# Performance work log

Hardware: AMD Instinct MI355X
Metric: run time of the kernel (lower is better)

## Reference

```python
import jax, jax.numpy as jnp
import numpy as np

D, DC, DR, NH = 2048, 512, 64, 16
HD = D // NH
B, T = 2, 2048


def _rope_tables(sl, off, dr):
    inv = 1.0 / (10000.0 ** (jnp.arange(0, dr, 2, dtype=jnp.float32) / dr))
    t = jnp.arange(off, off + sl, dtype=jnp.float32)
    f = jnp.outer(t, inv)                      # [sl, dr/2]
    e = jnp.concatenate([f, f], -1)            # [sl, dr]
    return jnp.cos(e), jnp.sin(e)


def _rap(x, c, s):
    d = x.shape[-1]
    x1, x2 = x[..., : d // 2], x[..., d // 2:]
    ch, sh = c[..., : d // 2], s[..., : d // 2]
    return jnp.concatenate([x1 * ch - x2 * sh, x2 * ch + x1 * sh], -1)


def setup_inputs() -> dict:
    key = jax.random.key(0)
    ks = jax.random.split(key, 8)
    def w(k, i, o):
        return jax.random.normal(k, (i, o), jnp.float32) * (1.0 / np.sqrt(i))
    return {
        "x": jax.random.normal(ks[0], (B, T, D), jnp.float32),
        "Wkv": w(ks[1], D, DC),    # kv_down
        "Wkup": w(ks[2], DC, D),   # k_up
        "Wvup": w(ks[3], DC, D),   # v_up
        "Wq": w(ks[4], D, D),      # q_proj
        "Wqr": w(ks[5], D, DR),    # q_rope
        "Wkr": w(ks[6], DC, DR),   # k_rope
        "Wo": w(ks[7], D, D),      # o_proj
    }


def reference(x, Wkv, Wkup, Wvup, Wq, Wqr, Wkr, Wo):
    Bx, Tx, d = x.shape
    offset = 0
    ckv = x @ Wkv                                   # [B,T,dc]
    kr = ckv @ Wkr                                  # [B,T,dr]
    cos, sin = _rope_tables(Tx, offset, DR)         # [T,dr]
    kr = _rap(kr, cos[None], sin[None])
    entry = jnp.concatenate([ckv, kr], -1)          # [B,T,dc+dr] (kv cache entry)
    tl = entry.shape[1]

    k = (ckv @ Wkup).reshape(Bx, tl, NH, HD).transpose(0, 2, 1, 3)   # [B,H,tl,hd]
    v = (ckv @ Wvup).reshape(Bx, tl, NH, HD).transpose(0, 2, 1, 3)
    q = (x @ Wq).reshape(Bx, Tx, NH, HD).transpose(0, 2, 1, 3)        # [B,H,T,hd]

    qr = _rap(x @ Wqr, cos[None], sin[None])        # [B,T,dr]

    ac = jnp.einsum("bhtd,bhsd->bhts", q, k)        # content scores
    ar = jnp.einsum("btd,bsd->bts", qr, kr)         # shared RoPE scores (same per head)
    scale = np.sqrt(HD + DR).astype(np.float32)
    scores = (ac + ar[:, None]) / scale             # [B,H,T,tl]

    # causal mask: triu(-inf, diagonal=tl-T+1)
    i = jnp.arange(Tx)[:, None]
    j = jnp.arange(tl)[None, :]
    mask = j > i + (tl - Tx)
    scores = jnp.where(mask[None, None], -jnp.inf, scores)

    attn = jax.nn.softmax(scores, -1)
    out = jnp.einsum("bhts,bhsd->bhtd", attn, v).transpose(0, 2, 1, 3).reshape(Bx, Tx, -1)
    return out @ Wo, entry
```

## Files before the change

### kernel.cpp

```cpp
#include <hip/hip_runtime.h>
#include <math.h>
#include <type_traits>

#define D    2048
#define DC   512
#define DR   64
#define NH   16
#define HD   128
#define Bb   2
#define Tt   2048
#define ROWS (Bb*Tt)
#define LDX  2176

typedef __bf16 bf16x8 __attribute__((ext_vector_type(8)));
typedef __bf16 bf16x4 __attribute__((ext_vector_type(4)));
typedef float  f32x4  __attribute__((ext_vector_type(4)));
typedef float  f32x16 __attribute__((ext_vector_type(16)));
typedef unsigned int uint;

typedef const void __attribute__((address_space(1))) gvoid;
typedef void       __attribute__((address_space(3))) lvoid;

__device__ __forceinline__ void load_lds16(const void* g, void* l) {
    __builtin_amdgcn_global_load_lds((gvoid*)g, (lvoid*)l, 16, 0, 0);
}

template <bool WF32, bool WBF16>
__global__ __launch_bounds__(256)
void gemm_bt(const __bf16* __restrict__ A, const __bf16* __restrict__ BT,
             float* __restrict__ Cf, __bf16* __restrict__ Cb,
             int M, int K, int ldcf, int ldcb) {
    __shared__ __bf16 As[128 * 32];
    __shared__ __bf16 Bs[128 * 32];

    const int tid  = threadIdx.x;
    const int w    = tid >> 6;
    const int lane = tid & 63;
    const int quad = lane >> 4;
    const int lc   = lane & 15;
    const int bm   = blockIdx.y * 128;
    const int bn   = blockIdx.x * 128;
    const int wm   = (w & 1) * 64;
    const int wn   = (w >> 1) * 64;

    const int sr = w * 32 + (lane >> 2);
    const int sc = (lane & 3) * 8;

    f32x4 acc[4][4] = {};

    for (int k0 = 0; k0 < K; k0 += 32) {
        const __bf16* ga = A  + (size_t)(bm + sr) * K + k0 + sc;
        const __bf16* gb = BT + (size_t)(bn + sr) * K + k0 + sc;
        load_lds16(ga,                  &As[(w * 32) * 32]);
        load_lds16(ga + (size_t)16 * K, &As[(w * 32 + 16) * 32]);
        load_lds16(gb,                  &Bs[(w * 32) * 32]);
        load_lds16(gb + (size_t)16 * K, &Bs[(w * 32 + 16) * 32]);
        __syncthreads();

        bf16x8 af[4], bfr[4];
        #pragma unroll
        for (int mi = 0; mi < 4; ++mi)
            af[mi] = *(bf16x8*)&As[(wm + mi * 16 + lc) * 32 + quad * 8];
        #pragma unroll
        for (int ni = 0; ni < 4; ++ni)
            bfr[ni] = *(bf16x8*)&Bs[(wn + ni * 16 + lc) * 32 + quad * 8];
        #pragma unroll
        for (int mi = 0; mi < 4; ++mi)
            #pragma unroll
            for (int ni = 0; ni < 4; ++ni)
                acc[mi][ni] = __builtin_amdgcn_mfma_f32_16x16x32_bf16(
                    af[mi], bfr[ni], acc[mi][ni], 0, 0, 0);
        __syncthreads();
    }

    #pragma unroll
    for (int mi = 0; mi < 4; ++mi)
        #pragma unroll
        for (int r = 0; r < 4; ++r) {
            const int row = bm + wm + mi * 16 + quad * 4 + r;
            const int col = bn + wn + lc;
            #pragma unroll
            for (int ni = 0; ni < 4; ++ni) {
                float v = acc[mi][ni][r];
                if constexpr (WF32)  Cf[(size_t)row * ldcf + col + ni * 16] = v;
                if constexpr (WBF16) Cb[(size_t)row * ldcb + col + ni * 16] = (__bf16)v;
            }
        }
}

__global__ void f32_to_bf16(const float* __restrict__ in,
                            __bf16* __restrict__ out, int n) {
    int i = blockIdx.x * blockDim.x + threadIdx.x;
    if (i < n) out[i] = (__bf16)in[i];
}

__global__ __launch_bounds__(256)
void transpose_conv(const float* __restrict__ W, __bf16* __restrict__ WT,
                    int R, int C) {
    __shared__ float tile[64][65];
    const int r0 = blockIdx.x * 64;
    const int c0 = blockIdx.y * 64;
    const int tid = threadIdx.x;
    for (int e = tid; e < 64 * 64; e += 256) {
        int i = e >> 6, j = e & 63;
        tile[i][j] = W[(size_t)(r0 + i) * C + c0 + j];
    }
    __syncthreads();
    for (int e = tid; e < 64 * 64; e += 256) {
        int i = e >> 6, j = e & 63;
        WT[(size_t)(c0 + i) * R + r0 + j] = (__bf16)tile[j][i];
    }
}

__global__ void rope_ext(__bf16* __restrict__ p, float* __restrict__ ent) {
    int idx = blockIdx.x * blockDim.x + threadIdx.x;
    if (idx >= ROWS * 32) return;
    int row = idx >> 5;
    int i   = idx & 31;
    int t   = row & (Tt - 1);
    float inv  = powf(10000.0f, -(float)(2 * i) / 64.0f);
    float fr   = (float)t * inv;
    float c = cosf(fr), s = sinf(fr);
    __bf16* v = p + (size_t)row * LDX + 2048;
    float x1 = (float)v[i], x2 = (float)v[i + 32];
    float o1 = x1 * c - x2 * s;
    float o2 = x2 * c + x1 * s;
    v[i]      = (__bf16)o1;
    v[i + 32] = (__bf16)o2;
    if (ent) {
        ent[(size_t)row * 576 + 512 + i] = o1;
        ent[(size_t)row * 576 + 544 + i] = o2;
    }
}

__global__ __launch_bounds__(256)
void transpose_v(const __bf16* __restrict__ vb, __bf16* __restrict__ vtb) {
    __shared__ __bf16 tile[64][65];
    const int t0 = blockIdx.x * 64;
    const int c0 = blockIdx.y * 64;
    const int b  = blockIdx.z;
    const int tid = threadIdx.x;
    for (int e = tid; e < 64 * 64; e += 256) {
        int i = e >> 6, j = e & 63;
        tile[i][j] = vb[((size_t)(b * Tt + t0 + i)) * D + c0 + j];
    }
    __syncthreads();
    for (int e = tid; e < 64 * 64; e += 256) {
        int i = e >> 6, j = e & 63;
        vtb[((size_t)(b * D + c0 + i)) * Tt + t0 + j] = tile[j][i];
    }
}

#define KS_STR 200
#define VT_STR 72
#define PS_STR 72
#define SPLIT_TILES 8

__device__ __forceinline__ int pbase_qt(int qt) {
    int a = qt >> 2, r = qt & 3;
    return qt + 2 * a * (a - 1) + r * a;
}

__global__ __launch_bounds__(256, 2)
void attn_split(const __bf16* __restrict__ qx, const __bf16* __restrict__ kx,
                const __bf16* __restrict__ vtb, __bf16* __restrict__ opart,
                float* __restrict__ mlpart) {
    const int qt = (Tt / 128 - 1) - (int)blockIdx.y;
    const int sp = blockIdx.x;
    const int t0 = sp * SPLIT_TILES;
    const int ntiles = 2 * qt + 2;
    if (t0 >= ntiles) return;
    const int tend = min(t0 + SPLIT_TILES, ntiles);
    const int hb = blockIdx.z;
    const int h  = hb & (NH - 1);
    const int b  = hb >> 4;
    const int q0 = qt * 128;

    __shared__ __bf16 Ks[64][KS_STR];
    __shared__ __bf16 Vt[128][VT_STR];
    __shared__ __bf16 PsT[4][32][PS_STR];

    const int tid    = threadIdx.x;
    const int w      = tid >> 6;
    const int lane   = tid & 63;
    const int lane31 = lane & 31;
    const int hi     = lane >> 5;
    const int hi8    = hi * 8;
    const int hi4    = hi * 4;

    const int qwmax = q0 + w * 32 + 31;
    const int tendw = min(tend, (qwmax >> 6) + 1);
    const int qglob = q0 + w * 32 + lane31;

    bf16x8 aq[12];
    {
        const __bf16* qrow = qx + (size_t)(b * Tt + q0 + w * 32 + lane31) * LDX;
        #pragma unroll
        for (int kt = 0; kt < 8; ++kt)
            aq[kt] = *(const bf16x8*)(qrow + h * HD + kt * 16 + hi8);
        #pragma unroll
        for (int kt = 0; kt < 4; ++kt)
            aq[8 + kt] = *(const bf16x8*)(qrow + 2048 + kt * 16 + hi8);
    }

    int krow[6], kcol[6], kgo[6];
    #pragma unroll
    for (int j = 0; j < 6; ++j) {
        int c   = tid + j * 256;
        int row = c / 24, c24 = c - row * 24;
        krow[j] = row;
        kcol[j] = c24 * 8;
        kgo[j]  = row * LDX + ((c24 < 16) ? (h * HD + c24 * 8)
                                          : (2048 + (c24 - 16) * 8));
    }
    const int vrow = tid >> 3;
    const int vcol = (tid & 7) * 8;
    const __bf16* kb0 = kx + (size_t)b * Tt * LDX;
    const __bf16* vb0 = vtb + ((size_t)b * D + (size_t)h * HD) * Tt;

    bf16x8 pk[6], pvv[4];
    {
        const __bf16* kbt = kb0 + (size_t)(t0 * 64) * LDX;
        const __bf16* vbt = vb0 + t0 * 64;
        #pragma unroll
        for (int j = 0; j < 6; ++j) pk[j] = *(const bf16x8*)(kbt + kgo[j]);
        #pragma unroll
        for (int j = 0; j < 4; ++j)
            pvv[j] = *(const bf16x8*)(vbt + (vrow + j * 32) * Tt + vcol);
    }

    float m_i = -1e30f, l_i = 0.f;
    f32x16 Of[4] = {};

    const float rscale = 0.07216878364870323f;

    for (int it = t0; it < tend; ++it) {
        const int s0 = it * 64;
        __syncthreads();
        #pragma unroll
        for (int j = 0; j < 6; ++j) *(bf16x8*)&Ks[krow[j]][kcol[j]] = pk[j];
        #pragma unroll
        for (int j = 0; j < 4; ++j) *(bf16x8*)&Vt[vrow + j * 32][vcol] = pvv[j];
        __syncthreads();

        if (it + 1 < tend) {
            const __bf16* kbn = kb0 + (size_t)(s0 + 64) * LDX;
            const __bf16* vbn = vb0 + (s0 + 64);
            #pragma unroll
            for (int j = 0; j < 6; ++j) pk[j] = *(const bf16x8*)(kbn + kgo[j]);
            #pragma unroll
            for (int j = 0; j < 4; ++j)
                pvv[j] = *(const bf16x8*)(vbn + (vrow + j * 32) * Tt + vcol);
        }

        if (it < tendw) {
            f32x16 st0 = {}, st1 = {};
            __builtin_amdgcn_s_setprio(1);
            #pragma unroll
            for (int kt = 0; kt < 12; ++kt) {
                bf16x8 ak0 = *(bf16x8*)&Ks[lane31][kt * 16 + hi8];
                bf16x8 ak1 = *(bf16x8*)&Ks[32 + lane31][kt * 16 + hi8];
                st0 = __builtin_amdgcn_mfma_f32_32x32x16_bf16(ak0, aq[kt], st0, 0, 0, 0);
                st1 = __builtin_amdgcn_mfma_f32_32x32x16_bf16(ak1, aq[kt], st1, 0, 0, 0);
            }
            __builtin_amdgcn_s_setprio(0);

            const bool dm = (s0 + 63 > q0 + w * 32);
            float sv0[16], sv1[16];
            float mt = -1e30f;
            #pragma unroll
            for (int r = 0; r < 16; ++r) {
                float a0 = st0[r] * rscale;
                float a1 = st1[r] * rscale;
                if (dm) {
                    int kr = (r & 3) + 8 * (r >> 2) + hi4;
                    if (s0 + kr > qglob)      a0 = -1e30f;
                    if (s0 + 32 + kr > qglob) a1 = -1e30f;
                }
                sv0[r] = a0; sv1[r] = a1;
                mt = fmaxf(mt, fmaxf(a0, a1));
            }
            mt = fmaxf(mt, __shfl_xor(mt, 32, 64));

            float mn = fmaxf(m_i, mt);
            float al = __expf(m_i - mn);
            m_i = mn;

            float rsum = 0.f;
            #pragma unroll
            for (int g = 0; g < 4; ++g) {
                bf16x4 pr;
                #pragma unroll
                for (int j = 0; j < 4; ++j) {
                    __bf16 pb = (__bf16)__expf(sv0[g * 4 + j] - mn);
                    pr[j] = pb;
                    rsum += (float)pb;
                }
                *(bf16x4*)&PsT[w][lane31][g * 8 + hi4] = pr;
            }
            #pragma unroll
            for (int g = 0; g < 4; ++g) {
                bf16x4 pr;
                #pragma unroll
                for (int j = 0; j < 4; ++j) {
                    __bf16 pb = (__bf16)__expf(sv1[g * 4 + j] - mn);
                    pr[j] = pb;
                    rsum += (float)pb;
                }
                *(bf16x4*)&PsT[w][lane31][32 + g * 8 + hi4] = pr;
            }
            rsum += __shfl_xor(rsum, 32, 64);
            l_i = l_i * al + rsum;
            #pragma unroll
            for (int nb = 0; nb < 4; ++nb) Of[nb] *= al;

            __builtin_amdgcn_s_setprio(1);
            #pragma unroll
            for (int kblk = 0; kblk < 4; ++kblk) {
                bf16x8 bp = *(bf16x8*)&PsT[w][lane31][kblk * 16 + hi8];
                #pragma unroll
                for (int nb = 0; nb < 4; ++nb) {
                    bf16x8 av = *(bf16x8*)&Vt[nb * 32 + lane31][kblk * 16 + hi8];
                    Of[nb] = __builtin_amdgcn_mfma_f32_32x32x16_bf16(av, bp, Of[nb], 0, 0, 0);
                }
            }
            __builtin_amdgcn_s_setprio(0);
        }
    }

    const int p = hb * 40 + pbase_qt(qt) + sp;
    __bf16* ob = opart + (size_t)p * (128 * 128) + (size_t)(w * 32 + lane31) * 128;
    #pragma unroll
    for (int nb = 0; nb < 4; ++nb)
        #pragma unroll
        for (int g = 0; g < 4; ++g) {
            bf16x4 o4;
            #pragma unroll
            for (int j = 0; j < 4; ++j) o4[j] = (__bf16)Of[nb][g * 4 + j];
            *(bf16x4*)(ob + nb * 32 + g * 8 + hi4) = o4;
        }
    if (hi == 0) {
        mlpart[(size_t)p * 256 + w * 32 + lane31]       = m_i;
        mlpart[(size_t)p * 256 + 128 + w * 32 + lane31] = l_i;
    }
}

__global__ __launch_bounds__(256)
void attn_reduce(const __bf16* __restrict__ opart, const float* __restrict__ mlpart,
                 __bf16* __restrict__ aob) {
    const int qt = blockIdx.x;
    const int hb = blockIdx.y;
    const int h  = hb & (NH - 1);
    const int b  = hb >> 4;
    const int nsp = (qt >> 2) + 1;
    const int p0  = hb * 40 + pbase_qt(qt);
    const int tid = threadIdx.x;
    const int ql  = tid >> 1;
    const int cg  = (tid & 1) * 64;

    float M = -1e30f;
    for (int s = 0; s < nsp; ++s)
        M = fmaxf(M, mlpart[(size_t)(p0 + s) * 256 + ql]);
    float L = 0.f;
    float acc[64];
    #pragma unroll
    for (int j = 0; j < 64; ++j) acc[j] = 0.f;
    for (int s = 0; s < nsp; ++s) {
        float ms = mlpart[(size_t)(p0 + s) * 256 + ql];
        float ls = mlpart[(size_t)(p0 + s) * 256 + 128 + ql];
        float sc = __expf(ms - M);
        L += ls * sc;
        const __bf16* op = opart + (size_t)(p0 + s) * (128 * 128) + (size_t)ql * 128 + cg;
        #pragma unroll
        for (int j8 = 0; j8 < 8; ++j8) {
            bf16x8 v = *(const bf16x8*)(op + j8 * 8);
            #pragma unroll
            for (int e = 0; e < 8; ++e) acc[j8 * 8 + e] += sc * (float)v[e];
        }
    }
    float invL = 1.0f / L;
    __bf16* outp = aob + ((size_t)(b * Tt + qt * 128 + ql)) * D + h * HD + cg;
    #pragma unroll
    for (int j8 = 0; j8 < 8; ++j8) {
        bf16x8 v;
        #pragma unroll
        for (int e = 0; e < 8; ++e) v[e] = (__bf16)(acc[j8 * 8 + e] * invL);
        *(bf16x8*)(outp + j8 * 8) = v;
    }
}

extern "C" void kernel_launch(void* const* d_in, const int* in_sizes, int n_in,
                              void* d_out, int out_size, void* d_ws, size_t ws_size,
                              hipStream_t stream) {
    const float* x    = (const float*)d_in[0];
    const float* Wkv  = (const float*)d_in[1];
    const float* Wkup = (const float*)d_in[2];
    const float* Wvup = (const float*)d_in[3];
    const float* Wq   = (const float*)d_in[4];
    const float* Wqr  = (const float*)d_in[5];
    const float* Wkr  = (const float*)d_in[6];
    const float* Wo   = (const float*)d_in[7];

    float* out0 = (float*)d_out;
    float* out1 = out0 + (size_t)ROWS * D;

    char* wsb = (char*)d_ws;
    __bf16* qext = (__bf16*)wsb;  wsb += (size_t)ROWS * LDX * 2;
    __bf16* kext = (__bf16*)wsb;  wsb += (size_t)ROWS * LDX * 2;
    __bf16* vtb  = (__bf16*)wsb;  wsb += (size_t)ROWS * D   * 2;
    __bf16* aob  = (__bf16*)wsb;  wsb += (size_t)ROWS * D   * 2;
    __bf16* WoT  = (__bf16*)wsb;  wsb += (size_t)D * D * 2;

    char* scratch = wsb;
    __bf16* xb    = (__bf16*)scratch;
    __bf16* vb    = (__bf16*)(scratch + 16777216);
    __bf16* ckvb  = (__bf16*)(scratch + 33554432);
    __bf16* WkvT  = (__bf16*)(scratch + 37748736);
    __bf16* WqxT  = (__bf16*)(scratch + 39845888);
    __bf16* KupxT = (__bf16*)(scratch + 48758784);
    __bf16* WvupT = (__bf16*)(scratch + 50987008);
    __bf16* opart  = (__bf16*)scratch;
    float*  mlpart = (float*)(scratch + (size_t)1280 * 128 * 128 * 2);

    dim3 blk(256);

    f32_to_bf16<<<(ROWS * D + 255) / 256, blk, 0, stream>>>(x, xb, ROWS * D);
    transpose_conv<<<dim3(D / 64, DC / 64), blk, 0, stream>>>(Wkv, WkvT, D, DC);
    transpose_conv<<<dim3(D / 64, D / 64),  blk, 0, stream>>>(Wq, WqxT, D, D);
    transpose_conv<<<dim3(D / 64, 1),       blk, 0, stream>>>(Wqr, WqxT + (size_t)D * D, D, DR);
    transpose_conv<<<dim3(DC / 64, D / 64), blk, 0, stream>>>(Wkup, KupxT, DC, D);
    transpose_conv<<<dim3(DC / 64, 1),      blk, 0, stream>>>(Wkr, KupxT + (size_t)D * DC, DC, DR);
    transpose_conv<<<dim3(DC / 64, D / 64), blk, 0, stream>>>(Wvup, WvupT, DC, D);
    transpose_conv<<<dim3(D / 64, D / 64),  blk, 0, stream>>>(Wo, WoT, D, D);

    gemm_bt<true, true><<<dim3(DC / 128, ROWS / 128), blk, 0, stream>>>(
        xb, WkvT, out1, ckvb, ROWS, D, 576, DC);

    gemm_bt<false, true><<<dim3(LDX / 128, ROWS / 128), blk, 0, stream>>>(
        xb, WqxT, (float*)nullptr, qext, ROWS, D, 0, LDX);
    rope_ext<<<(ROWS * 32 + 255) / 256, blk, 0, stream>>>(qext, (float*)nullptr);

    gemm_bt<false, true><<<dim3(LDX / 128, ROWS / 128), blk, 0, stream>>>(
        ckvb, KupxT, (float*)nullptr, kext, ROWS, DC, 0, LDX);
    rope_ext<<<(ROWS * 32 + 255) / 256, blk, 0, stream>>>(kext, out1);

    gemm_bt<false, true><<<dim3(D / 128, ROWS / 128), blk, 0, stream>>>(
        ckvb, WvupT, (float*)nullptr, vb, ROWS, DC, 0, D);
    transpose_v<<<dim3(Tt / 64, D / 64, Bb), blk, 0, stream>>>(vb, vtb);

    attn_split<<<dim3(4, Tt / 128, NH * Bb), blk, 0, stream>>>(
        qext, kext, vtb, opart, mlpart);
    attn_reduce<<<dim3(Tt / 128, NH * Bb), blk, 0, stream>>>(opart, mlpart, aob);

    gemm_bt<true, false><<<dim3(D / 128, ROWS / 128), blk, 0, stream>>>(
        aob, WoT, out0, (__bf16*)nullptr, ROWS, D, D, 0);
}
```

Before: 527.5 us.

## Halve P staging buffer, raise attention occupancy, and swizzle block order for locality

```diff
diff --git a/kernel.cpp b/kernel.cpp
--- a/kernel.cpp
+++ b/kernel.cpp
@@ -33,13 +33,20 @@
     __shared__ __bf16 As[128 * 32];
     __shared__ __bf16 Bs[128 * 32];
 
+    const int nx   = gridDim.x;
+    const int lin  = (int)(blockIdx.x + nx * blockIdx.y);
+    const int chunk = (nx * gridDim.y) >> 3;
+    const int nid  = (lin & 7) * chunk + (lin >> 3);
+    const int bxs  = nid % nx;
+    const int bys  = nid / nx;
+
     const int tid  = threadIdx.x;
     const int w    = tid >> 6;
     const int lane = tid & 63;
     const int quad = lane >> 4;
     const int lc   = lane & 15;
-    const int bm   = blockIdx.y * 128;
-    const int bn   = blockIdx.x * 128;
+    const int bm   = bys * 128;
+    const int bn   = bxs * 128;
     const int wm   = (w & 1) * 64;
     const int wn   = (w >> 1) * 64;
 
@@ -153,7 +160,7 @@
 
 #define KS_STR 200
 #define VT_STR 72
-#define PS_STR 72
+#define PS_STR 36
 #define SPLIT_TILES 8
 
 __device__ __forceinline__ int pbase_qt(int qt) {
@@ -161,17 +168,20 @@
     return qt + 2 * a * (a - 1) + r * a;
 }
 
-__global__ __launch_bounds__(256, 2)
+__global__ __launch_bounds__(256, 3)
 void attn_split(const __bf16* __restrict__ qx, const __bf16* __restrict__ kx,
                 const __bf16* __restrict__ vtb, __bf16* __restrict__ opart,
                 float* __restrict__ mlpart) {
-    const int qt = (Tt / 128 - 1) - (int)blockIdx.y;
-    const int sp = blockIdx.x;
+    const int lin = (int)(blockIdx.x + (blockIdx.y << 2) + (blockIdx.z << 6));
+    const int nid = ((lin & 7) << 8) + (lin >> 3);
+    const int sp  = nid & 3;
+    const int qt  = (Tt / 128 - 1) - ((nid >> 2) & 15);
+    const int hb  = nid >> 6;
+
     const int t0 = sp * SPLIT_TILES;
     const int ntiles = 2 * qt + 2;
     if (t0 >= ntiles) return;
     const int tend = min(t0 + SPLIT_TILES, ntiles);
-    const int hb = blockIdx.z;
     const int h  = hb & (NH - 1);
     const int b  = hb >> 4;
     const int q0 = qt * 128;
@@ -285,8 +295,11 @@
             float mn = fmaxf(m_i, mt);
             float al = __expf(m_i - mn);
             m_i = mn;
+            #pragma unroll
+            for (int nb = 0; nb < 4; ++nb) Of[nb] *= al;
 
             float rsum = 0.f;
+
             #pragma unroll
             for (int g = 0; g < 4; ++g) {
                 bf16x4 pr;
@@ -298,6 +311,18 @@
                 }
                 *(bf16x4*)&PsT[w][lane31][g * 8 + hi4] = pr;
             }
+            __builtin_amdgcn_s_setprio(1);
+            #pragma unroll
+            for (int kblk = 0; kblk < 2; ++kblk) {
+                bf16x8 bp = *(bf16x8*)&PsT[w][lane31][kblk * 16 + hi8];
+                #pragma unroll
+                for (int nb = 0; nb < 4; ++nb) {
+                    bf16x8 av = *(bf16x8*)&Vt[nb * 32 + lane31][kblk * 16 + hi8];
+                    Of[nb] = __builtin_amdgcn_mfma_f32_32x32x16_bf16(av, bp, Of[nb], 0, 0, 0);
+                }
+            }
+            __builtin_amdgcn_s_setprio(0);
+
             #pragma unroll
             for (int g = 0; g < 4; ++g) {
                 bf16x4 pr;
@@ -307,24 +332,22 @@
                     pr[j] = pb;
                     rsum += (float)pb;
                 }
-                *(bf16x4*)&PsT[w][lane31][32 + g * 8 + hi4] = pr;
-            }
-            rsum += __shfl_xor(rsum, 32, 64);
-            l_i = l_i * al + rsum;
-            #pragma unroll
-            for (int nb = 0; nb < 4; ++nb) Of[nb] *= al;
-
+                *(bf16x4*)&PsT[w][lane31][g * 8 + hi4] = pr;
+            }
             __builtin_amdgcn_s_setprio(1);
             #pragma unroll
-            for (int kblk = 0; kblk < 4; ++kblk) {
+            for (int kblk = 0; kblk < 2; ++kblk) {
                 bf16x8 bp = *(bf16x8*)&PsT[w][lane31][kblk * 16 + hi8];
                 #pragma unroll
                 for (int nb = 0; nb < 4; ++nb) {
-                    bf16x8 av = *(bf16x8*)&Vt[nb * 32 + lane31][kblk * 16 + hi8];
+                    bf16x8 av = *(bf16x8*)&Vt[nb * 32 + lane31][(2 + kblk) * 16 + hi8];
                     Of[nb] = __builtin_amdgcn_mfma_f32_32x32x16_bf16(av, bp, Of[nb], 0, 0, 0);
                 }
             }
             __builtin_amdgcn_s_setprio(0);
+
+            rsum += __shfl_xor(rsum, 32, 64);
+            l_i = l_i * al + rsum;
         }
     }
 
```

After: 615.0 us. +16.6%, slower.
